# Optimization experiments

Measured on AMD Instinct MI355X. Metric: run time of the kernel, lower is better.

The kernel has to match this reference:

```python
import jax, jax.numpy as jnp
import numpy as np
from jax.scipy.linalg import cho_solve

D, A, H, N, T = 64, 8, 256, 16, 128
DT = 0.05
# GPR hyperparameters set_hyperparameter(0.1, 0.1, 0.1): lengthscale, signal std, noise std
L2, SF2, SN2 = 0.1 ** 2, 0.1 ** 2, 0.1 ** 2


def _rbf(t1, t2):
    # t1: (P,), t2: (Q,) -> (P, Q) squared-exponential kernel
    d2 = (t1[:, None] - t2[None, :]) ** 2
    return SF2 * jnp.exp(-0.5 * d2 / L2)


def _gp_predict(t, y, tq):
    # t, y: (N,) training inputs/targets; tq: (T,) query times
    K = _rbf(t, t) + SN2 * jnp.eye(t.shape[0], dtype=t.dtype)
    Ks = _rbf(tq, t)          # (T, N)
    Kss = _rbf(tq, tq)        # (T, T)
    Lc = jnp.linalg.cholesky(K)
    alpha = cho_solve((Lc, True), y)        # (N,)
    V = cho_solve((Lc, True), Ks.T)         # (N, T)
    mu = Ks @ alpha                          # (T,)
    cov = Kss - Ks @ V                       # (T, T)
    return mu, cov


def setup_inputs() -> dict:
    key = jax.random.key(0)
    ks = jax.random.split(key, 8)
    def lin(k, out_d, in_d):
        return (jax.random.normal(k, (out_d, in_d), jnp.float32) / np.sqrt(in_d).astype(np.float32))
    return {
        "x": jax.random.normal(ks[0], (512, D), jnp.float32),
        "a": jax.random.normal(ks[1], (512, A), jnp.float32),
        "da": jax.random.normal(ks[2], (512, A), jnp.float32),
        "W1": lin(ks[3], H, D), "b1": jnp.zeros((H,), jnp.float32),
        "W2": lin(ks[4], H, H), "b2": jnp.zeros((H,), jnp.float32),
        "Wt": lin(ks[5], N, H), "bt": jnp.zeros((N,), jnp.float32),
        "Wa": lin(ks[6], N * A, H), "ba": jnp.zeros((N * A,), jnp.float32),
        "time_array": jnp.arange(1, T + 1, dtype=jnp.float32) * DT,
    }


def reference(x, a, da, W1, b1, W2, b2, Wt, bt, Wa, ba, time_array):
    E = x.shape[0]
    h = jnp.tanh(x @ W1.T + b1)
    h = jnp.tanh(h @ W2.T + b2)
    times = h @ Wt.T + bt                              # (E, N)
    anchors = (h @ Wa.T + ba).reshape(E, A, N)         # (E, A, N)
    ts = jnp.broadcast_to(times[:, None, :], (E, A, N)).reshape(E * A, N)
    ys = anchors.reshape(E * A, N)
    mu, cov = jax.vmap(lambda t, y: _gp_predict(t, y, time_array))(ts, ys)
    return mu.reshape(E, A, T), cov.reshape(E, A, T, T)
```

## Files before the change

kernel.cpp:

```cpp
#include <hip/hip_runtime.h>

#define Ecnt 512
#define Dd 64
#define Aa 8
#define Hh 256
#define Nn 16
#define Tt 128
#define SF2c 0.01f
#define SN2c 0.01f
#define NEGHALF_INV_L2 (-50.0f)

__device__ __forceinline__ float dotrow(const float* __restrict__ w, const float* v, int n4) {
    const float4* w4 = (const float4*)w;
    float acc = 0.f;
    #pragma unroll 8
    for (int k = 0; k < n4; ++k) {
        float4 q = w4[k];
        acc += q.x * v[4*k+0];
        acc += q.y * v[4*k+1];
        acc += q.z * v[4*k+2];
        acc += q.w * v[4*k+3];
    }
    return acc;
}

__global__ __launch_bounds__(256, 2) void grp_kernel(
    const float* __restrict__ x,
    const float* __restrict__ W1, const float* __restrict__ b1,
    const float* __restrict__ W2, const float* __restrict__ b2,
    const float* __restrict__ Wt, const float* __restrict__ bt,
    const float* __restrict__ Wa, const float* __restrict__ ba,
    const float* __restrict__ tarr,
    float* __restrict__ out_mu, float* __restrict__ out_cov)
{
    const int e   = blockIdx.x;
    const int tid = threadIdx.x;

    __shared__ float xs[Dd];
    __shared__ float h1[Hh];
    __shared__ float h2[Hh];
    __shared__ float tt[Nn];
    __shared__ float tq[Tt];
    __shared__ float yy[Aa][Nn];
    __shared__ float Km[Nn][Nn + 1];
    __shared__ float Lm[Nn][Nn + 1];
    __shared__ float tmpv[Nn];
    __shared__ __align__(16) float Ks[Tt][Nn];
    __shared__ __align__(16) float V[Nn][Tt];
    __shared__ float alpha[Aa][Nn];

    if (tid < Dd) xs[tid] = x[e * Dd + tid];
    if (tid < Tt) tq[tid] = tarr[tid];
    __syncthreads();

    h1[tid] = tanhf(b1[tid] + dotrow(W1 + tid * Dd, xs, Dd / 4));
    __syncthreads();
    h2[tid] = tanhf(b2[tid] + dotrow(W2 + tid * Hh, h1, Hh / 4));
    __syncthreads();

    if (tid < Nn) {
        tt[tid] = bt[tid] + dotrow(Wt + tid * Hh, h2, Hh / 4);
    } else if (tid < Nn + Aa * Nn) {
        int r = tid - Nn;
        float v = ba[r] + dotrow(Wa + r * Hh, h2, Hh / 4);
        yy[r >> 4][r & 15] = v;
    }
    __syncthreads();

    {
        int i = tid >> 4, j = tid & 15;
        float d = tt[i] - tt[j];
        Km[i][j] = SF2c * __expf(NEGHALF_INV_L2 * d * d) + (i == j ? SN2c : 0.f);
    }
    #pragma unroll
    for (int r = 0; r < 8; ++r) {
        int idx = tid + r * 256;
        int q = idx >> 4, i = idx & 15;
        float d = tq[q] - tt[i];
        Ks[q][i] = SF2c * __expf(NEGHALF_INV_L2 * d * d);
    }
    __syncthreads();

    for (int j = 0; j < Nn; ++j) {
        if (tid >= j && tid < Nn) {
            float s = Km[tid][j];
            for (int k = 0; k < j; ++k) s -= Lm[tid][k] * Lm[j][k];
            tmpv[tid] = s;
        }
        __syncthreads();
        if (tid >= j && tid < Nn) {
            float dj = sqrtf(tmpv[j]);
            Lm[tid][j] = (tid == j) ? dj : tmpv[tid] / dj;
        }
        __syncthreads();
    }

    if (tid < Tt + Aa) {
        float bz[Nn];
        if (tid < Tt) {
            float tqv = tq[tid];
            #pragma unroll
            for (int i = 0; i < Nn; ++i) {
                float d = tqv - tt[i];
                bz[i] = SF2c * __expf(NEGHALF_INV_L2 * d * d);
            }
        } else {
            int a = tid - Tt;
            #pragma unroll
            for (int i = 0; i < Nn; ++i) bz[i] = yy[a][i];
        }
        #pragma unroll
        for (int i = 0; i < Nn; ++i) {
            float s = bz[i];
            for (int k = 0; k < i; ++k) s -= Lm[i][k] * bz[k];
            bz[i] = s / Lm[i][i];
        }
        #pragma unroll
        for (int i = Nn - 1; i >= 0; --i) {
            float s = bz[i];
            for (int k = i + 1; k < Nn; ++k) s -= Lm[k][i] * bz[k];
            bz[i] = s / Lm[i][i];
        }
        if (tid < Tt) {
            #pragma unroll
            for (int i = 0; i < Nn; ++i) V[i][tid] = bz[i];
        } else {
            int a = tid - Tt;
            #pragma unroll
            for (int i = 0; i < Nn; ++i) alpha[a][i] = bz[i];
        }
    }
    __syncthreads();

    if (tid < Tt) {
        float ks[Nn];
        #pragma unroll
        for (int i = 0; i < Nn; ++i) ks[i] = Ks[tid][i];
        size_t mb = (size_t)e * (Aa * Tt) + tid;
        #pragma unroll
        for (int a = 0; a < Aa; ++a) {
            float m = 0.f;
            #pragma unroll
            for (int i = 0; i < Nn; ++i) m += ks[i] * alpha[a][i];
            out_mu[mb + (size_t)a * Tt] = m;
        }
    }

    {
        const int q4 = (tid & 31) * 4;
        const int pg = tid >> 5;
        float vq[Nn][4];
        #pragma unroll
        for (int i = 0; i < Nn; ++i) {
            float4 vv = *(const float4*)&V[i][q4];
            vq[i][0] = vv.x; vq[i][1] = vv.y; vq[i][2] = vv.z; vq[i][3] = vv.w;
        }
        const float tqq0 = tq[q4 + 0], tqq1 = tq[q4 + 1], tqq2 = tq[q4 + 2], tqq3 = tq[q4 + 3];
        float* covb = out_cov + (size_t)e * (Aa * Tt * Tt);
        #pragma unroll
        for (int pp = 0; pp < 16; ++pp) {
            const int p = pg * 16 + pp;
            float ksp[Nn];
            #pragma unroll
            for (int i4 = 0; i4 < 4; ++i4) {
                float4 kv = *(const float4*)&Ks[p][i4 * 4];
                ksp[i4*4+0] = kv.x; ksp[i4*4+1] = kv.y; ksp[i4*4+2] = kv.z; ksp[i4*4+3] = kv.w;
            }
            const float tqp = tq[p];
            float d0 = tqp - tqq0, d1 = tqp - tqq1, d2 = tqp - tqq2, d3 = tqp - tqq3;
            float a0 = SF2c * __expf(NEGHALF_INV_L2 * d0 * d0);
            float a1 = SF2c * __expf(NEGHALF_INV_L2 * d1 * d1);
            float a2 = SF2c * __expf(NEGHALF_INV_L2 * d2 * d2);
            float a3 = SF2c * __expf(NEGHALF_INV_L2 * d3 * d3);
            #pragma unroll
            for (int i = 0; i < Nn; ++i) {
                a0 -= ksp[i] * vq[i][0];
                a1 -= ksp[i] * vq[i][1];
                a2 -= ksp[i] * vq[i][2];
                a3 -= ksp[i] * vq[i][3];
            }
            float4 pk;
            pk.x = a0; pk.y = a1; pk.z = a2; pk.w = a3;
            const size_t ro = (size_t)p * Tt + q4;
            #pragma unroll
            for (int a = 0; a < Aa; ++a) {
                *(float4*)(covb + (size_t)a * (Tt * Tt) + ro) = pk;
            }
        }
    }
}

extern "C" void kernel_launch(void* const* d_in, const int* in_sizes, int n_in,
                              void* d_out, int out_size, void* d_ws, size_t ws_size,
                              hipStream_t stream) {
    (void)in_sizes; (void)n_in; (void)out_size; (void)d_ws; (void)ws_size;
    const float* x  = (const float*)d_in[0];
    const float* W1 = (const float*)d_in[3];
    const float* b1 = (const float*)d_in[4];
    const float* W2 = (const float*)d_in[5];
    const float* b2 = (const float*)d_in[6];
    const float* Wt = (const float*)d_in[7];
    const float* bt = (const float*)d_in[8];
    const float* Wa = (const float*)d_in[9];
    const float* ba = (const float*)d_in[10];
    const float* ta = (const float*)d_in[11];
    float* mu  = (float*)d_out;
    float* cov = mu + (size_t)Ecnt * Aa * Tt;
    grp_kernel<<<Ecnt, 256, 0, stream>>>(x, W1, b1, W2, b2, Wt, bt, Wa, ba, ta, mu, cov);
}
```

Before: 312.0 us.

## Split covariance write into compute kernel plus separate replication kernel

The fused kernel now writes one covariance matrix per sample to workspace, and a second kernel reads it back and writes the eight identical copies to the output. The aim is to keep the heavy compute kernel from stalling on a large store stream and to let a simple high-occupancy copy kernel saturate write bandwidth. In exchange it adds an extra global round trip (write plus read of 32 MB), a second launch, and a dependence on the workspace being large enough.

```diff
diff --git a/kernel.cpp b/kernel.cpp
--- a/kernel.cpp
+++ b/kernel.cpp
@@ -24,14 +24,14 @@
     return acc;
 }
 
-__global__ __launch_bounds__(256, 2) void grp_kernel(
+__global__ __launch_bounds__(256, 2) void grp_compute(
     const float* __restrict__ x,
     const float* __restrict__ W1, const float* __restrict__ b1,
     const float* __restrict__ W2, const float* __restrict__ b2,
     const float* __restrict__ Wt, const float* __restrict__ bt,
     const float* __restrict__ Wa, const float* __restrict__ ba,
     const float* __restrict__ tarr,
-    float* __restrict__ out_mu, float* __restrict__ out_cov)
+    float* __restrict__ out_mu, float* __restrict__ ws_cov)
 {
     const int e   = blockIdx.x;
     const int tid = threadIdx.x;
@@ -156,7 +156,7 @@
             vq[i][0] = vv.x; vq[i][1] = vv.y; vq[i][2] = vv.z; vq[i][3] = vv.w;
         }
         const float tqq0 = tq[q4 + 0], tqq1 = tq[q4 + 1], tqq2 = tq[q4 + 2], tqq3 = tq[q4 + 3];
-        float* covb = out_cov + (size_t)e * (Aa * Tt * Tt);
+        float* covb = ws_cov + (size_t)e * (Tt * Tt);
         #pragma unroll
         for (int pp = 0; pp < 16; ++pp) {
             const int p = pg * 16 + pp;
@@ -179,21 +179,39 @@
                 a2 -= ksp[i] * vq[i][2];
                 a3 -= ksp[i] * vq[i][3];
             }
-            float4 pk;
-            pk.x = a0; pk.y = a1; pk.z = a2; pk.w = a3;
-            const size_t ro = (size_t)p * Tt + q4;
-            #pragma unroll
-            for (int a = 0; a < Aa; ++a) {
-                *(float4*)(covb + (size_t)a * (Tt * Tt) + ro) = pk;
-            }
-        }
+            float4 pk; pk.x = a0; pk.y = a1; pk.z = a2; pk.w = a3;
+            *(float4*)(covb + (size_t)p * Tt + q4) = pk;
+        }
+    }
+}
+
+__global__ __launch_bounds__(256, 4) void grp_replicate(
+    const float* __restrict__ ws_cov, float* __restrict__ out_cov)
+{
+    const int b  = blockIdx.x;
+    const int e  = b >> 2;
+    const int qr = b & 3;
+    const int t  = threadIdx.x;
+    const float4* src = (const float4*)(ws_cov + (size_t)e * (Tt * Tt) + qr * (32 * Tt));
+    float4* dstb = (float4*)(out_cov + (size_t)e * (Aa * Tt * Tt) + qr * (32 * Tt));
+    float4 v0 = src[t + 0 * 256];
+    float4 v1 = src[t + 1 * 256];
+    float4 v2 = src[t + 2 * 256];
+    float4 v3 = src[t + 3 * 256];
+    #pragma unroll
+    for (int a = 0; a < Aa; ++a) {
+        float4* dst = dstb + (size_t)a * (Tt * Tt / 4);
+        dst[t + 0 * 256] = v0;
+        dst[t + 1 * 256] = v1;
+        dst[t + 2 * 256] = v2;
+        dst[t + 3 * 256] = v3;
     }
 }
 
 extern "C" void kernel_launch(void* const* d_in, const int* in_sizes, int n_in,
                               void* d_out, int out_size, void* d_ws, size_t ws_size,
                               hipStream_t stream) {
-    (void)in_sizes; (void)n_in; (void)out_size; (void)d_ws; (void)ws_size;
+    (void)in_sizes; (void)n_in; (void)out_size; (void)ws_size;
     const float* x  = (const float*)d_in[0];
     const float* W1 = (const float*)d_in[3];
     const float* b1 = (const float*)d_in[4];
@@ -206,5 +224,7 @@
     const float* ta = (const float*)d_in[11];
     float* mu  = (float*)d_out;
     float* cov = mu + (size_t)Ecnt * Aa * Tt;
-    grp_kernel<<<Ecnt, 256, 0, stream>>>(x, W1, b1, W2, b2, Wt, bt, Wa, ba, ta, mu, cov);
-}
+    float* wsc = (float*)d_ws;
+    grp_compute<<<Ecnt, 256, 0, stream>>>(x, W1, b1, W2, b2, Wt, bt, Wa, ba, ta, mu, wsc);
+    grp_replicate<<<Ecnt * 4, 256, 0, stream>>>(wsc, cov);
+}
```

Result: slower. 342.4 us (+9.7%).
